# Optimization experiments

Hardware: AMD Instinct MI355X
Metric: run time of the kernel (lower is better)

The kernel has to match this reference:

```python
import jax, jax.numpy as jnp
import numpy as np

L, D, H, B, S, V = 4, 1024, 16, 8, 512, 32000
DK = D // H          # per-head dim = 64; only head 0 is ever used (bug in source)
FF = 4 * D
EPS = 1e-3           # keras BatchNormalization default epsilon


def _bn(x, gamma, beta, mean, var):
    # inference-mode BatchNorm over last axis (keras default)
    return gamma * (x - mean) * jax.lax.rsqrt(var + EPS) + beta


def setup_inputs() -> dict:
    key = jax.random.key(0)
    keys = iter(jax.random.split(key, 40))

    def rn(shape, scale=0.02):
        return jax.random.normal(next(keys), shape, jnp.float32) * scale

    sequence = jax.random.randint(next(keys), (B, S), 0, V, dtype=jnp.int32)

    # standard sinusoidal positional encoding table [S, D]
    pos = np.arange(S)[:, None].astype(np.float32)
    i = np.arange(D)[None, :]
    angle = pos / np.power(10000.0, (2 * (i // 2)) / D).astype(np.float32)
    pes = np.where(i % 2 == 0, np.sin(angle), np.cos(angle)).astype(np.float32)

    return {
        "sequence": sequence,
        "emb": rn((V, D)),
        "pes": jnp.asarray(pes),
        # single-head attention params (head 0 only, per the source bug), stacked over layers
        "wq": rn((L, D, DK)), "bq": jnp.zeros((L, DK)),
        "wk": rn((L, D, DK)), "bk": jnp.zeros((L, DK)),
        "wv": rn((L, D, DK)), "bv": jnp.zeros((L, DK)),
        "wo": rn((L, DK, D)), "bo": jnp.zeros((L, D)),
        "att_gamma": 1.0 + rn((L, D), 0.1), "att_beta": rn((L, D), 0.1),
        "att_mean": rn((L, D), 0.1), "att_var": jnp.ones((L, D)),
        "w1": rn((L, D, FF)), "bff1": jnp.zeros((L, FF)),
        "w2": rn((L, FF, D)), "bff2": jnp.zeros((L, D)),
        "ffn_gamma": 1.0 + rn((L, D), 0.1), "ffn_beta": rn((L, D), 0.1),
        "ffn_mean": rn((L, D), 0.1), "ffn_var": jnp.ones((L, D)),
    }


def reference(sequence, emb, pes, wq, bq, wk, bk, wv, bv, wo, bo,
              att_gamma, att_beta, att_mean, att_var,
              w1, bff1, w2, bff2,
              ffn_gamma, ffn_beta, ffn_mean, ffn_var):
    # embedding + positional bug: only pes[i, 0] (a scalar per position) is added
    x = emb[sequence] + pes[:S, 0:1][None]          # [B, S, D]
    scale = 1.0 / jnp.sqrt(jnp.float32(DK))
    for l in range(L):
        q = x @ wq[l] + bq[l]                       # [B, S, DK]
        k = x @ wk[l] + bk[l]
        v = x @ wv[l] + bv[l]
        score = jnp.einsum('bqd,bkd->bqk', q, k) * scale
        head = jax.nn.softmax(score, axis=-1) @ v   # [B, S, DK]
        att = head @ wo[l] + bo[l]                  # [B, S, D]
        x = _bn(x + att, att_gamma[l], att_beta[l], att_mean[l], att_var[l])
        ffn = jax.nn.relu(x @ w1[l] + bff1[l]) @ w2[l] + bff2[l]
        x = _bn(x + ffn, ffn_gamma[l], ffn_beta[l], ffn_mean[l], ffn_var[l])
    return x
```

## Files before the change

kernel.cpp:

```cpp
#include <hip/hip_runtime.h>
#include <hip/hip_bf16.h>
#include <stdint.h>

#define L_  4
#define D_  1024
#define DK_ 64
#define B_  8
#define S_  512
#define FF_ 4096
#define M_  (B_*S_)
#define EPS_ 1e-3f
#define QKVN_ 256

typedef __bf16 bf16_t;
typedef bf16_t bf16x8 __attribute__((ext_vector_type(8)));
typedef float  f32x4  __attribute__((ext_vector_type(4)));

__device__ __forceinline__ bf16_t f2b(float f) {
    union { float f; uint32_t u; } v; v.f = f;
    uint32_t r = v.u + 0x7fff + ((v.u >> 16) & 1);
    uint16_t h = (uint16_t)(r >> 16);
    bf16_t o; __builtin_memcpy(&o, &h, 2); return o;
}

__device__ __forceinline__ void gl2lds16(const bf16_t* g, bf16_t* l) {
    __builtin_amdgcn_global_load_lds(
        (__attribute__((address_space(1))) void*)g,
        (__attribute__((address_space(3))) void*)l, 16, 0, 0);
}

__global__ void embed_kernel(const int* __restrict__ seq, const float* __restrict__ emb,
                             const float* __restrict__ pes, float* __restrict__ x,
                             bf16_t* __restrict__ xb) {
    int idx = blockIdx.x * 256 + threadIdx.x;
    int md  = idx >> 10;
    int d   = idx & (D_ - 1);
    int s   = md & (S_ - 1);
    float v = emb[(size_t)seq[md] * D_ + d] + pes[s * D_];
    x[idx] = v;
    xb[idx] = f2b(v);
}

__device__ __forceinline__ void tile_tr(const float* __restrict__ src, bf16_t* __restrict__ dst,
                                        int K, int N, int kb, int nb, float (*t)[33]) {
    int k0 = kb * 32, n0 = nb * 32;
    int c = threadIdx.x & 31, r = threadIdx.x >> 5;
    #pragma unroll
    for (int i = 0; i < 4; i++)
        t[r + i * 8][c] = src[(size_t)(k0 + r + i * 8) * N + n0 + c];
    __syncthreads();
    #pragma unroll
    for (int i = 0; i < 4; i++)
        dst[(size_t)(n0 + r + i * 8) * K + k0 + c] = f2b(t[c][r + i * 8]);
}

__global__ void prep_weights(const float* __restrict__ wq, const float* __restrict__ wk,
                             const float* __restrict__ wv, const float* __restrict__ wo,
                             const float* __restrict__ w1, const float* __restrict__ w2,
                             const float* __restrict__ bq, const float* __restrict__ bk,
                             const float* __restrict__ bv,
                             bf16_t* __restrict__ wqkvt, bf16_t* __restrict__ wot,
                             bf16_t* __restrict__ w1t, bf16_t* __restrict__ w2t,
                             float* __restrict__ bqkv) {
    __shared__ float t[32][33];
    int bid = blockIdx.x;
    if (bid < 4096) {
        tile_tr(w1, w1t, D_, FF_, bid & 31, bid >> 5, t);
    } else if (bid < 8192) {
        int rem = bid - 4096;
        tile_tr(w2, w2t, FF_, D_, rem & 127, rem >> 7, t);
    } else if (bid < 8384) {
        int rem = bid - 8192;
        int which = rem >> 6; rem &= 63;
        const float* src = which == 0 ? wq : (which == 1 ? wk : wv);
        tile_tr(src, wqkvt + (size_t)which * 64 * D_, D_, DK_, rem & 31, rem >> 5, t);
    } else if (bid < 8448) {
        int rem = bid - 8384;
        tile_tr(wo, wot, DK_, D_, rem & 1, rem >> 1, t);
    } else if (bid < 8464) {
        int rem = bid - 8448;
        bf16_t* z = wqkvt + (size_t)192 * D_ + rem * 4096;
        for (int i = threadIdx.x; i < 4096; i += 256) z[i] = (bf16_t)0.f;
    } else {
        int n = threadIdx.x;
        float v = 0.f;
        if      (n <  64) v = bq[n];
        else if (n < 128) v = bk[n - 64];
        else if (n < 192) v = bv[n - 128];
        bqkv[n] = v;
    }
}

template<int MODE>
__global__ __launch_bounds__(256)
void gemm_mfma3(const bf16_t* __restrict__ A, const bf16_t* __restrict__ Bt,
                const float* __restrict__ bias, bf16_t* __restrict__ Cb,
                const float* __restrict__ Xin, float* __restrict__ Xf, bf16_t* __restrict__ Xb,
                const float* __restrict__ g, const float* __restrict__ bb,
                const float* __restrict__ mu, const float* __restrict__ var,
                int N, int K, int kChunk, size_t strideZ) {
    __shared__ bf16_t As[128 * 64];
    __shared__ bf16_t Bs[128 * 64];
    const int tid  = threadIdx.x;
    const int w    = tid >> 6, lane = tid & 63;
    const int wm   = w >> 1,   wn   = w & 1;
    const int lm   = lane & 15, quad = lane >> 4;
    const int m0 = blockIdx.y * 128, n0 = blockIdx.x * 128;
    const int kBeg = blockIdx.z * kChunk, kEnd = kBeg + kChunk;
    const int lrow = lane >> 3;
    const int lk   = (lane & 7) ^ lrow;

    f32x4 acc[4][4];
    #pragma unroll
    for (int i = 0; i < 4; i++)
        #pragma unroll
        for (int j = 0; j < 4; j++) acc[i][j] = (f32x4){0.f, 0.f, 0.f, 0.f};

    for (int k0 = kBeg; k0 < kEnd; k0 += 64) {
        #pragma unroll
        for (int i = 0; i < 4; i++) {
            const int r0 = w * 32 + i * 8;
            gl2lds16(A  + (size_t)(m0 + r0 + lrow) * K + k0 + lk * 8, As + r0 * 64);
            gl2lds16(Bt + (size_t)(n0 + r0 + lrow) * K + k0 + lk * 8, Bs + r0 * 64);
        }
        __syncthreads();
        #pragma unroll
        for (int s = 0; s < 2; s++) {
            bf16x8 af[4], bfr[4];
            #pragma unroll
            for (int mi = 0; mi < 4; mi++) {
                const int ra = wm * 64 + mi * 16 + lm;
                af[mi] = *(const bf16x8*)(As + ra * 64 + (((s * 4 + quad) ^ (lm & 7)) * 8));
            }
            #pragma unroll
            for (int ni = 0; ni < 4; ni++) {
                const int rb = wn * 64 + ni * 16 + lm;
                bfr[ni] = *(const bf16x8*)(Bs + rb * 64 + (((s * 4 + quad) ^ (lm & 7)) * 8));
            }
            #pragma unroll
            for (int mi = 0; mi < 4; mi++)
                #pragma unroll
                for (int ni = 0; ni < 4; ni++)
                    acc[mi][ni] = __builtin_amdgcn_mfma_f32_16x16x32_bf16(
                        af[mi], bfr[ni], acc[mi][ni], 0, 0, 0);
        }
        __syncthreads();
    }

    bf16_t* Pz = (MODE == 2) ? Cb + (size_t)blockIdx.z * strideZ : Cb;

    #pragma unroll
    for (int ni = 0; ni < 4; ni++) {
        const int col = n0 + wn * 64 + ni * 16 + lm;
        float bv = 0.f, gv = 0.f, bbv = 0.f, muv = 0.f, rsv = 0.f;
        if (MODE != 2) bv = bias[col];
        if (MODE == 3) {
            gv = g[col]; bbv = bb[col]; muv = mu[col];
            rsv = rsqrtf(var[col] + EPS_);
        }
        #pragma unroll
        for (int mi = 0; mi < 4; mi++) {
            const int rbase = m0 + wm * 64 + mi * 16 + quad * 4;
            #pragma unroll
            for (int r = 0; r < 4; r++) {
                const size_t idx = (size_t)(rbase + r) * N + col;
                float v = acc[mi][ni][r] + bv;
                if (MODE == 1) Cb[idx] = f2b(fmaxf(v, 0.f));
                if (MODE == 2) Pz[idx] = f2b(v);
                if (MODE == 3) {
                    float s = Xin[idx] + v;
                    float o = gv * (s - muv) * rsv + bbv;
                    Xf[idx] = o;
                    Xb[idx] = f2b(o);
                }
            }
        }
    }
}

__global__ void qkv_reduce(const bf16_t* __restrict__ P, const float* __restrict__ bias,
                           bf16_t* __restrict__ dst) {
    int idx = blockIdx.x * 256 + threadIdx.x;
    int n = idx & (QKVN_ - 1);
    float s = bias[n];
    #pragma unroll
    for (int zz = 0; zz < 4; zz++) s += (float)P[(size_t)zz * M_ * QKVN_ + idx];
    dst[idx] = f2b(s);
}

__global__ void vt_kernel(const bf16_t* __restrict__ qkv, bf16_t* __restrict__ Vt) {
    int b = blockIdx.y, k0 = blockIdx.x * 64;
    const bf16_t* vb = qkv + (size_t)b * S_ * QKVN_ + 128;
    __shared__ bf16_t t[64][65];
    int c = threadIdx.x & 63, r4 = threadIdx.x >> 6;
    #pragma unroll
    for (int i = 0; i < 16; i++) {
        int k = i * 4 + r4;
        t[c][k] = vb[(size_t)(k0 + k) * QKVN_ + c];
    }
    __syncthreads();
    #pragma unroll
    for (int i = 0; i < 16; i++) {
        int d = i * 4 + r4;
        Vt[((size_t)b * DK_ + d) * S_ + k0 + c] = t[d][c];
    }
}

__global__ __launch_bounds__(256)
void attn_fused(const bf16_t* __restrict__ qkv, const bf16_t* __restrict__ Vt,
                bf16_t* __restrict__ hdb) {
    const int b  = blockIdx.y;
    const int i0 = blockIdx.x * 64;
    const bf16_t* qb  = qkv + (size_t)b * S_ * QKVN_;
    const bf16_t* kb  = qb + 64;
    const bf16_t* vtb = Vt + (size_t)b * DK_ * S_;

    __shared__ bf16_t Ps[8 * 64 * 64];
    __shared__ bf16_t Vs[8 * 64 * 64];
    __shared__ float  rowred[4][64];

    const int tid  = threadIdx.x;
    const int w    = tid >> 6, lane = tid & 63;
    const int lm   = lane & 15, quad = lane >> 4;
    const int lrow = lane >> 3;
    const int lk   = (lane & 7) ^ lrow;

    #pragma unroll
    for (int i = 0; i < 16; i++) {
        const int r0 = w * 16 + (i & 1) * 8;
        const int kt = i >> 1;
        gl2lds16(vtb + (size_t)(r0 + lrow) * S_ + kt * 64 + lk * 8,
                 Vs + kt * 4096 + r0 * 64);
    }

    f32x4 acc[4][8];
    #pragma unroll
    for (int mi = 0; mi < 4; mi++)
        #pragma unroll
        for (int ni = 0; ni < 8; ni++) acc[mi][ni] = (f32x4){0.f, 0.f, 0.f, 0.f};

    #pragma unroll
    for (int s = 0; s < 2; s++) {
        bf16x8 af[4], bfr[8];
        #pragma unroll
        for (int mi = 0; mi < 4; mi++)
            af[mi] = *(const bf16x8*)(qb + (size_t)(i0 + mi * 16 + lm) * QKVN_ + s * 32 + quad * 8);
        #pragma unroll
        for (int ni = 0; ni < 8; ni++)
            bfr[ni] = *(const bf16x8*)(kb + (size_t)(w * 128 + ni * 16 + lm) * QKVN_ + s * 32 + quad * 8);
        #pragma unroll
        for (int mi = 0; mi < 4; mi++)
            #pragma unroll
            for (int ni = 0; ni < 8; ni++)
                acc[mi][ni] = __builtin_amdgcn_mfma_f32_16x16x32_bf16(
                    af[mi], bfr[ni], acc[mi][ni], 0, 0, 0);
    }
    #pragma unroll
    for (int mi = 0; mi < 4; mi++)
        #pragma unroll
        for (int ni = 0; ni < 8; ni++) acc[mi][ni] *= 0.125f;

    float rmax[4][4];
    #pragma unroll
    for (int mi = 0; mi < 4; mi++)
        #pragma unroll
        for (int r = 0; r < 4; r++) {
            float m = acc[mi][0][r];
            #pragma unroll
            for (int ni = 1; ni < 8; ni++) m = fmaxf(m, acc[mi][ni][r]);
            #pragma unroll
            for (int off = 1; off < 16; off <<= 1) m = fmaxf(m, __shfl_xor(m, off, 64));
            rmax[mi][r] = m;
        }
    if (lm == 0) {
        #pragma unroll
        for (int mi = 0; mi < 4; mi++)
            #pragma unroll
            for (int r = 0; r < 4; r++)
                rowred[w][mi * 16 + quad * 4 + r] = rmax[mi][r];
    }
    __syncthreads();
    float gmax[4][4];
    #pragma unroll
    for (int mi = 0; mi < 4; mi++)
        #pragma unroll
        for (int r = 0; r < 4; r++) {
            const int row = mi * 16 + quad * 4 + r;
            gmax[mi][r] = fmaxf(fmaxf(rowred[0][row], rowred[1][row]),
                                fmaxf(rowred[2][row], rowred[3][row]));
        }
    __syncthreads();

    float rsum[4][4];
    #pragma unroll
    for (int mi = 0; mi < 4; mi++)
        #pragma unroll
        for (int r = 0; r < 4; r++) rsum[mi][r] = 0.f;
    #pragma unroll
    for (int mi = 0; mi < 4; mi++) {
        #pragma unroll
        for (int ni = 0; ni < 8; ni++) {
            const int key = w * 128 + ni * 16 + lm;
            const int kt  = key >> 6;
            const int ck  = (key >> 3) & 7;
            #pragma unroll
            for (int r = 0; r < 4; r++) {
                const int m = mi * 16 + quad * 4 + r;
                float p = __expf(acc[mi][ni][r] - gmax[mi][r]);
                bf16_t pb = f2b(p);
                rsum[mi][r] += (float)pb;
                Ps[kt * 4096 + m * 64 + ((ck ^ (m & 7)) * 8) + (key & 7)] = pb;
            }
        }
    }
    #pragma unroll
    for (int mi = 0; mi < 4; mi++)
        #pragma unroll
        for (int r = 0; r < 4; r++) {
            float s = rsum[mi][r];
            #pragma unroll
            for (int off = 1; off < 16; off <<= 1) s += __shfl_xor(s, off, 64);
            rsum[mi][r] = s;
        }
    if (lm == 0) {
        #pragma unroll
        for (int mi = 0; mi < 4; mi++)
            #pragma unroll
            for (int r = 0; r < 4; r++)
                rowred[w][mi * 16 + quad * 4 + r] = rsum[mi][r];
    }
    __syncthreads();

    f32x4 accO[4];
    #pragma unroll
    for (int ni = 0; ni < 4; ni++) accO[ni] = (f32x4){0.f, 0.f, 0.f, 0.f};
    #pragma unroll
    for (int ks = 0; ks < 16; ks++) {
        const int kt = ks >> 1;
        const int co = (ks & 1) * 4 + quad;
        bf16x8 af = *(const bf16x8*)(Ps + kt * 4096 + (w * 16 + lm) * 64 + ((co ^ (lm & 7)) * 8));
        #pragma unroll
        for (int ni = 0; ni < 4; ni++) {
            bf16x8 bfr = *(const bf16x8*)(Vs + kt * 4096 + (ni * 16 + lm) * 64 + ((co ^ (lm & 7)) * 8));
            accO[ni] = __builtin_amdgcn_mfma_f32_16x16x32_bf16(af, bfr, accO[ni], 0, 0, 0);
        }
    }

    #pragma unroll
    for (int r = 0; r < 4; r++) {
        const int row = w * 16 + quad * 4 + r;
        const float tot = rowred[0][row] + rowred[1][row] + rowred[2][row] + rowred[3][row];
        const float inv = 1.0f / tot;
        #pragma unroll
        for (int ni = 0; ni < 4; ni++)
            hdb[(size_t)(b * S_ + i0 + row) * DK_ + ni * 16 + lm] = f2b(accO[ni][r] * inv);
    }
}

__global__ void bn_residual2(const float* __restrict__ x, const bf16_t* __restrict__ p,
                             const float* __restrict__ bias,
                             const float* __restrict__ g, const float* __restrict__ b,
                             const float* __restrict__ mu, const float* __restrict__ var,
                             float* __restrict__ dst, bf16_t* __restrict__ dstb) {
    int idx = blockIdx.x * 256 + threadIdx.x;
    int d = idx & (D_ - 1);
    float r = bias[d] + (float)p[idx] + (float)p[(size_t)M_ * D_ + idx];
    float s = x[idx] + r;
    float o = g[d] * (s - mu[d]) * rsqrtf(var[d] + EPS_) + b[d];
    dst[idx] = o;
    dstb[idx] = f2b(o);
}

extern "C" void kernel_launch(void* const* d_in, const int* in_sizes, int n_in,
                              void* d_out, int out_size, void* d_ws, size_t ws_size,
                              hipStream_t stream) {
    const int*   seq = (const int*)  d_in[0];
    const float* emb = (const float*)d_in[1];
    const float* pes = (const float*)d_in[2];
    const float* wq  = (const float*)d_in[3];
    const float* bq  = (const float*)d_in[4];
    const float* wk  = (const float*)d_in[5];
    const float* bk  = (const float*)d_in[6];
    const float* wv  = (const float*)d_in[7];
    const float* bv  = (const float*)d_in[8];
    const float* wo  = (const float*)d_in[9];
    const float* bo  = (const float*)d_in[10];
    const float* ag  = (const float*)d_in[11];
    const float* ab  = (const float*)d_in[12];
    const float* am  = (const float*)d_in[13];
    const float* av  = (const float*)d_in[14];
    const float* w1  = (const float*)d_in[15];
    const float* b1  = (const float*)d_in[16];
    const float* w2  = (const float*)d_in[17];
    const float* b2  = (const float*)d_in[18];
    const float* fg  = (const float*)d_in[19];
    const float* fb  = (const float*)d_in[20];
    const float* fm  = (const float*)d_in[21];
    const float* fv  = (const float*)d_in[22];
    float* out = (float*)d_out;

    char* p = (char*)d_ws;
    auto alloc = [&](size_t bytes) { char* q = p; p += (bytes + 255) & ~(size_t)255; return q; };
    float*  X     = (float*) alloc((size_t)M_ * D_ * 4);
    bf16_t* Xb    = (bf16_t*)alloc((size_t)M_ * D_ * 2);
    bf16_t* qkvb  = (bf16_t*)alloc((size_t)M_ * QKVN_ * 2);
    bf16_t* Vtb   = (bf16_t*)alloc((size_t)B_ * DK_ * S_ * 2);
    bf16_t* hdb   = (bf16_t*)alloc((size_t)M_ * DK_ * 2);
    bf16_t* hb    = (bf16_t*)alloc((size_t)M_ * FF_ * 2);
    bf16_t* w1t   = (bf16_t*)alloc((size_t)FF_ * D_ * 2);
    bf16_t* w2t   = (bf16_t*)alloc((size_t)D_ * FF_ * 2);
    bf16_t* wqkvt = (bf16_t*)alloc((size_t)QKVN_ * D_ * 2);
    bf16_t* wot   = (bf16_t*)alloc((size_t)D_ * DK_ * 2);
    float*  bqkv  = (float*) alloc(QKVN_ * 4);

    embed_kernel<<<M_ * D_ / 256, 256, 0, stream>>>(seq, emb, pes, X, Xb);

    for (int l = 0; l < L_; l++) {
        prep_weights<<<8465, 256, 0, stream>>>(
            wq + (size_t)l * D_ * DK_, wk + (size_t)l * D_ * DK_, wv + (size_t)l * D_ * DK_,
            wo + (size_t)l * DK_ * D_, w1 + (size_t)l * D_ * FF_, w2 + (size_t)l * FF_ * D_,
            bq + l * DK_, bk + l * DK_, bv + l * DK_,
            wqkvt, wot, w1t, w2t, bqkv);

        gemm_mfma3<2><<<dim3(QKVN_ / 128, M_ / 128, 4), 256, 0, stream>>>(
            Xb, wqkvt, nullptr, (bf16_t*)out, nullptr, nullptr, nullptr,
            nullptr, nullptr, nullptr, nullptr, QKVN_, D_, D_ / 4, (size_t)M_ * QKVN_);
        qkv_reduce<<<M_ * QKVN_ / 256, 256, 0, stream>>>((const bf16_t*)out, bqkv, qkvb);

        vt_kernel<<<dim3(S_ / 64, B_), 256, 0, stream>>>(qkvb, Vtb);
        attn_fused<<<dim3(S_ / 64, B_), 256, 0, stream>>>(qkvb, Vtb, hdb);

        gemm_mfma3<3><<<dim3(D_ / 128, M_ / 128, 1), 256, 0, stream>>>(
            hdb, wot, bo + l * D_, nullptr, X, X, Xb,
            ag + l * D_, ab + l * D_, am + l * D_, av + l * D_, D_, DK_, DK_, 0);

        gemm_mfma3<1><<<dim3(FF_ / 128, M_ / 128, 1), 256, 0, stream>>>(
            Xb, w1t, b1 + l * FF_, hb, nullptr, nullptr, nullptr,
            nullptr, nullptr, nullptr, nullptr, FF_, D_, D_, 0);

        gemm_mfma3<2><<<dim3(D_ / 128, M_ / 128, 2), 256, 0, stream>>>(
            hb, w2t, nullptr, (bf16_t*)out, nullptr, nullptr, nullptr,
            nullptr, nullptr, nullptr, nullptr, D_, FF_, FF_ / 2, (size_t)M_ * D_);

        bn_residual2<<<M_ * D_ / 256, 256, 0, stream>>>(
            X, (const bf16_t*)out, b2 + l * D_,
            fg + l * D_, fb + l * D_, fm + l * D_, fv + l * D_, X, Xb);
        if (l == L_ - 1)
            hipMemcpyAsync(out, X, (size_t)M_ * D_ * 4, hipMemcpyDeviceToDevice, stream);
    }
}
```

Measured before the change: 919.3 us.

## Add 256x256 eight-phase pipelined MFMA GEMM for FFN layers

Adds a new 512-thread GEMM kernel with 256x256 output tiles, double-buffered LDS staging and an eight-phase schedule. Each phase interleaves global-to-LDS loads with half-tile MFMA bursts at raised priority. Both FFN GEMMs now use it. The second FFN GEMM uses a 4-way split-K into a new partials buffer, summed by a widened BN-residual kernel. The larger tiles aim to raise data reuse and overlap memory with compute, but they add register pressure and many barriers, and the extra split-K partials add memory traffic.

```diff
diff --git a/kernel.cpp b/kernel.cpp
--- a/kernel.cpp
+++ b/kernel.cpp
@@ -165,7 +165,6 @@
             for (int r = 0; r < 4; r++) {
                 const size_t idx = (size_t)(rbase + r) * N + col;
                 float v = acc[mi][ni][r] + bv;
-                if (MODE == 1) Cb[idx] = f2b(fmaxf(v, 0.f));
                 if (MODE == 2) Pz[idx] = f2b(v);
                 if (MODE == 3) {
                     float s = Xin[idx] + v;
@@ -178,6 +177,150 @@
     }
 }
 
+template<int MODE>
+__global__ __launch_bounds__(512, 2)
+void gemm_8ph(const bf16_t* __restrict__ A, const bf16_t* __restrict__ Bt,
+              const float* __restrict__ bias, bf16_t* __restrict__ Cb,
+              int N, int K, int kChunk, size_t strideZ) {
+    __shared__ bf16_t As[2][256 * 64];
+    __shared__ bf16_t Bs[2][256 * 64];
+    const int tid  = threadIdx.x;
+    const int w    = tid >> 6, lane = tid & 63;
+    const int wm   = w >> 2,   wn   = w & 3;
+    const int lm   = lane & 15, quad = lane >> 4;
+    const int m0 = blockIdx.y * 256, n0 = blockIdx.x * 256;
+    const int kBeg = blockIdx.z * kChunk;
+    const int lrow = lane >> 3;
+    const int lk   = (lane & 7) ^ lrow;
+    const int niter = kChunk >> 7;
+
+    f32x4 acc[8][4];
+    #pragma unroll
+    for (int i = 0; i < 8; i++)
+        #pragma unroll
+        for (int j = 0; j < 4; j++) acc[i][j] = (f32x4){0.f, 0.f, 0.f, 0.f};
+
+    auto stageA = [&](int buf, int half, int tile) {
+        const int kt0 = kBeg + tile * 64;
+        #pragma unroll
+        for (int j = 0; j < 2; j++) {
+            const int r0 = half * 128 + w * 16 + j * 8;
+            gl2lds16(A + (size_t)(m0 + r0 + lrow) * K + kt0 + lk * 8, &As[buf][r0 * 64]);
+        }
+    };
+    auto stageB = [&](int buf, int half, int tile) {
+        const int kt0 = kBeg + tile * 64;
+        #pragma unroll
+        for (int j = 0; j < 2; j++) {
+            const int r0 = half * 128 + w * 16 + j * 8;
+            gl2lds16(Bt + (size_t)(n0 + r0 + lrow) * K + kt0 + lk * 8, &Bs[buf][r0 * 64]);
+        }
+    };
+
+    bf16x8 af[8], bfr[4];
+    auto ldFrags = [&](int buf, int kk) {
+        #pragma unroll
+        for (int mi = 0; mi < 8; mi++) {
+            const int ra = wm * 128 + mi * 16 + lm;
+            af[mi] = *(const bf16x8*)(&As[buf][ra * 64 + (((kk * 4 + quad) ^ (lm & 7)) * 8)]);
+        }
+        #pragma unroll
+        for (int ni = 0; ni < 4; ni++) {
+            const int rb = wn * 64 + ni * 16 + lm;
+            bfr[ni] = *(const bf16x8*)(&Bs[buf][rb * 64 + (((kk * 4 + quad) ^ (lm & 7)) * 8)]);
+        }
+    };
+    auto mfmaHalf = [&](int mh) {
+        __builtin_amdgcn_s_setprio(1);
+        #pragma unroll
+        for (int mi = mh * 4; mi < mh * 4 + 4; mi++)
+            #pragma unroll
+            for (int ni = 0; ni < 4; ni++)
+                acc[mi][ni] = __builtin_amdgcn_mfma_f32_16x16x32_bf16(
+                    af[mi], bfr[ni], acc[mi][ni], 0, 0, 0);
+        __builtin_amdgcn_s_setprio(0);
+    };
+
+    stageA(0, 0, 0); stageA(0, 1, 0); stageB(0, 0, 0); stageB(0, 1, 0);
+    stageA(1, 0, 1);
+    asm volatile("s_waitcnt vmcnt(2)" ::: "memory");
+    __builtin_amdgcn_sched_barrier(0);
+    __builtin_amdgcn_s_barrier();
+
+    for (int i = 0; i < niter; i++) {
+        const int t0 = 2 * i;
+        const bool nl = (i < niter - 1);
+        ldFrags(0, 0);
+        stageA(1, 1, t0 + 1);
+        __builtin_amdgcn_s_barrier();
+        mfmaHalf(0);
+        __builtin_amdgcn_s_barrier();
+        stageB(1, 0, t0 + 1);
+        __builtin_amdgcn_s_barrier();
+        mfmaHalf(1);
+        __builtin_amdgcn_s_barrier();
+        ldFrags(0, 1);
+        stageB(1, 1, t0 + 1);
+        __builtin_amdgcn_s_barrier();
+        mfmaHalf(0);
+        __builtin_amdgcn_s_barrier();
+        if (nl) {
+            stageA(0, 0, t0 + 2);
+            asm volatile("s_waitcnt vmcnt(2)" ::: "memory");
+        } else {
+            asm volatile("s_waitcnt vmcnt(0)" ::: "memory");
+        }
+        __builtin_amdgcn_sched_barrier(0);
+        __builtin_amdgcn_s_barrier();
+        mfmaHalf(1);
+        __builtin_amdgcn_s_barrier();
+        ldFrags(1, 0);
+        if (nl) stageA(0, 1, t0 + 2);
+        __builtin_amdgcn_s_barrier();
+        mfmaHalf(0);
+        __builtin_amdgcn_s_barrier();
+        if (nl) stageB(0, 0, t0 + 2);
+        __builtin_amdgcn_s_barrier();
+        mfmaHalf(1);
+        __builtin_amdgcn_s_barrier();
+        ldFrags(1, 1);
+        if (nl) stageB(0, 1, t0 + 2);
+        __builtin_amdgcn_s_barrier();
+        mfmaHalf(0);
+        __builtin_amdgcn_s_barrier();
+        if (nl) {
+            stageA(1, 0, t0 + 3);
+            asm volatile("s_waitcnt vmcnt(2)" ::: "memory");
+        } else {
+            asm volatile("s_waitcnt vmcnt(0)" ::: "memory");
+        }
+        __builtin_amdgcn_sched_barrier(0);
+        __builtin_amdgcn_s_barrier();
+        mfmaHalf(1);
+        __builtin_amdgcn_s_barrier();
+    }
+
+    bf16_t* Pz = (MODE == 2) ? Cb + (size_t)blockIdx.z * strideZ : Cb;
+
+    #pragma unroll
+    for (int ni = 0; ni < 4; ni++) {
+        const int col = n0 + wn * 64 + ni * 16 + lm;
+        float bv = 0.f;
+        if (MODE == 1) bv = bias[col];
+        #pragma unroll
+        for (int mi = 0; mi < 8; mi++) {
+            const int rbase = m0 + wm * 128 + mi * 16 + quad * 4;
+            #pragma unroll
+            for (int r = 0; r < 4; r++) {
+                const size_t idx = (size_t)(rbase + r) * N + col;
+                float v = acc[mi][ni][r] + bv;
+                if (MODE == 1) Cb[idx] = f2b(fmaxf(v, 0.f));
+                if (MODE == 2) Pz[idx] = f2b(v);
+            }
+        }
+    }
+}
+
 __global__ void qkv_reduce(const bf16_t* __restrict__ P, const float* __restrict__ bias,
                            bf16_t* __restrict__ dst) {
     int idx = blockIdx.x * 256 + threadIdx.x;
@@ -357,14 +500,15 @@
     }
 }
 
-__global__ void bn_residual2(const float* __restrict__ x, const bf16_t* __restrict__ p,
+__global__ void bn_residual4(const float* __restrict__ x, const bf16_t* __restrict__ p,
                              const float* __restrict__ bias,
                              const float* __restrict__ g, const float* __restrict__ b,
                              const float* __restrict__ mu, const float* __restrict__ var,
                              float* __restrict__ dst, bf16_t* __restrict__ dstb) {
     int idx = blockIdx.x * 256 + threadIdx.x;
     int d = idx & (D_ - 1);
-    float r = bias[d] + (float)p[idx] + (float)p[(size_t)M_ * D_ + idx];
+    float r = bias[d] + (float)p[idx] + (float)p[(size_t)M_ * D_ + idx]
+            + (float)p[2 * (size_t)M_ * D_ + idx] + (float)p[3 * (size_t)M_ * D_ + idx];
     float s = x[idx] + r;
     float o = g[d] * (s - mu[d]) * rsqrtf(var[d] + EPS_) + b[d];
     dst[idx] = o;
@@ -411,6 +555,7 @@
     bf16_t* w2t   = (bf16_t*)alloc((size_t)D_ * FF_ * 2);
     bf16_t* wqkvt = (bf16_t*)alloc((size_t)QKVN_ * D_ * 2);
     bf16_t* wot   = (bf16_t*)alloc((size_t)D_ * DK_ * 2);
+    bf16_t* part  = (bf16_t*)alloc((size_t)4 * M_ * D_ * 2);
     float*  bqkv  = (float*) alloc(QKVN_ * 4);
 
     embed_kernel<<<M_ * D_ / 256, 256, 0, stream>>>(seq, emb, pes, X, Xb);
@@ -434,16 +579,14 @@
             hdb, wot, bo + l * D_, nullptr, X, X, Xb,
             ag + l * D_, ab + l * D_, am + l * D_, av + l * D_, D_, DK_, DK_, 0);
 
-        gemm_mfma3<1><<<dim3(FF_ / 128, M_ / 128, 1), 256, 0, stream>>>(
-            Xb, w1t, b1 + l * FF_, hb, nullptr, nullptr, nullptr,
-            nullptr, nullptr, nullptr, nullptr, FF_, D_, D_, 0);
-
-        gemm_mfma3<2><<<dim3(D_ / 128, M_ / 128, 2), 256, 0, stream>>>(
-            hb, w2t, nullptr, (bf16_t*)out, nullptr, nullptr, nullptr,
-            nullptr, nullptr, nullptr, nullptr, D_, FF_, FF_ / 2, (size_t)M_ * D_);
-
-        bn_residual2<<<M_ * D_ / 256, 256, 0, stream>>>(
-            X, (const bf16_t*)out, b2 + l * D_,
+        gemm_8ph<1><<<dim3(FF_ / 256, M_ / 256, 1), 512, 0, stream>>>(
+            Xb, w1t, b1 + l * FF_, hb, FF_, D_, D_, 0);
+
+        gemm_8ph<2><<<dim3(D_ / 256, M_ / 256, 4), 512, 0, stream>>>(
+            hb, w2t, nullptr, part, D_, FF_, FF_ / 4, (size_t)M_ * D_);
+
+        bn_residual4<<<M_ * D_ / 256, 256, 0, stream>>>(
+            X, part, b2 + l * D_,
             fg + l * D_, fb + l * D_, fm + l * D_, fv + l * D_, X, Xb);
         if (l == L_ - 1)
             hipMemcpyAsync(out, X, (size_t)M_ * D_ * 4, hipMemcpyDeviceToDevice, stream);
```

Measured after the change: 934.7 us. About the same (+1.7%).
